# Optimization experiments

Measured on AMD Instinct MI355X. Metric: run time of the kernel, lower is better.

Reference implementation:

```python
import jax, jax.numpy as jnp
import numpy as np

K = 5            # adaptive kernel size
C = 256          # inplanes
M = 4
CM = C // M      # 64 bottleneck channels
PLANES = 256


def _depthwise_per_sample(f, w, b, dilation, pad):
    # f: [N, Cm, H, W]; w: [N, Cm, kh, kw] per-sample depthwise weights; b: [Cm]
    # Fold batch into the channel/group dim so one grouped conv does all samples.
    N, Cm, H, W = f.shape
    x = f.reshape(1, N * Cm, H, W)
    wk = w.reshape(N * Cm, 1, w.shape[2], w.shape[3])
    out = jax.lax.conv_general_dilated(
        x, wk, window_strides=(1, 1), padding=[(pad, pad), (pad, pad)],
        rhs_dilation=(dilation, dilation), feature_group_count=N * Cm,
        dimension_numbers=("NCHW", "OIHW", "NCHW"))
    return out.reshape(N, Cm, H, W) + b[None, :, None, None]


def setup_inputs() -> dict:
    key = jax.random.key(0)
    ks = jax.random.split(key, 16)
    N, H, W = 16, 96, 96
    s = 0.05
    return {
        "x": jax.random.normal(ks[0], (N, C, H, W), jnp.float32),
        "conv_w": jax.random.normal(ks[1], (CM, C)) * s,            # 1x1 conv C->Cm
        "conv_b": jax.random.normal(ks[2], (CM,)) * s,
        "conv_k_w": jax.random.normal(ks[3], ()) * s + 1.0,          # conv_k: 1x1, 1ch
        "conv_k_b": jax.random.normal(ks[4], ()) * s,
        "conv_k2_w": jax.random.normal(ks[5], ()) * s + 1.0,         # conv_k2
        "conv_k2_b": jax.random.normal(ks[6], ()) * s,
        "conv_kernel_w": jax.random.normal(ks[7], (K * K,)) * s,     # 1 -> k*k
        "conv_kernel_b": jax.random.normal(ks[8], (K * K,)) * s,
        "conv_kernel2_w": jax.random.normal(ks[9], (9,)) * s,        # 1 -> 9
        "conv_kernel2_b": jax.random.normal(ks[10], (9,)) * s,
        "fuse_w": jax.random.normal(ks[11], (PLANES // 2, CM)) * s,  # 1x1 fuse
        "fuse_b": jax.random.normal(ks[12], (PLANES // 2,)) * s,
        "adap_b": jax.random.normal(ks[13], (CM,)) * s,              # conv_adap_kernel.bias
        "atrous_b": jax.random.normal(ks[14], (CM,)) * s,            # conv3x3_atrous bias
    }


def reference(x, conv_w, conv_b, conv_k_w, conv_k_b, conv_k2_w, conv_k2_b,
              conv_kernel_w, conv_kernel_b, conv_kernel2_w, conv_kernel2_b,
              fuse_w, fuse_b, adap_b, atrous_b):
    N = x.shape[0]
    # f = relu(1x1 conv)
    f = jax.nn.relu(jnp.einsum("oc,nchw->nohw", conv_w, x) + conv_b[None, :, None, None])
    # g = relu(conv(avg_pool(x))) -> [N, Cm]
    g = jax.nn.relu(x.mean(axis=(2, 3)) @ conv_w.T + conv_b)
    # conv_kernel (1->k*k, 1x1) applied over the Cm "spatial" axis, then conv_k (scalar affine)
    # kernel[n,c,kk] = conv_k_w * (conv_kernel_w[kk]*g[n,c] + conv_kernel_b[kk]) + conv_k_b
    ker = conv_k_w * (g[:, :, None] * conv_kernel_w[None, None, :] + conv_kernel_b) + conv_k_b
    w_dyn = ker.reshape(N, CM, K, K)
    ker2 = conv_k2_w * (g[:, :, None] * conv_kernel2_w[None, None, :] + conv_kernel2_b) + conv_k2_b
    w_atr = ker2.reshape(N, CM, 3, 3)
    # per-sample dynamic depthwise convs
    out = _depthwise_per_sample(f, w_dyn, adap_b, dilation=1, pad=(K - 1) // 2)
    out_atr = _depthwise_per_sample(f, w_atr, atrous_b, dilation=2, pad=2)
    # fuse (1x1) each branch, concat on channels
    y = jnp.einsum("oc,nchw->nohw", fuse_w, out) + fuse_b[None, :, None, None]
    y_atr = jnp.einsum("oc,nchw->nohw", fuse_w, out_atr) + fuse_b[None, :, None, None]
    return jnp.concatenate([y, y_atr], axis=1)
```

## Files before the change

kernel.cpp:

```cpp
#include <hip/hip_runtime.h>
#include <hip/hip_bf16.h>
#include <stdint.h>

#define N_S   16
#define C_IN  256
#define CMID  64
#define HH    96
#define WW    96
#define HW    9216
#define PL2   128

#define CB_OFF   0
#define KW_OFF   64
#define KB_OFF   96
#define K2W_OFF  128
#define K2B_OFF  144
#define FB_OFF   160
#define AB_OFF   288
#define ATB_OFF  352
#define SC_OFF   416

typedef __attribute__((ext_vector_type(8))) short short8;
typedef __attribute__((ext_vector_type(4))) float floatx4;

__device__ __forceinline__ float ldbf(const uint16_t* p) {
    return __uint_as_float(((uint32_t)(*p)) << 16);
}
__device__ __forceinline__ uint16_t f2bf(float f) {
    __hip_bfloat16 h = __float2bfloat16(f);
    return *reinterpret_cast<uint16_t*>(&h);
}
__device__ __forceinline__ uint32_t pkbf(float lo, float hi) {
    return (uint32_t)f2bf(lo) | ((uint32_t)f2bf(hi) << 16);
}
__device__ __forceinline__ float bfsum2(uint32_t u) {
    return __uint_as_float(u << 16) + __uint_as_float(u & 0xffff0000u);
}

#define SWZ8(row) ((((row) ^ ((row) >> 3)) & 7) << 3)

__global__ __launch_bounds__(256) void k_prep(
    const uint16_t* __restrict__ xq,
    const void* conv_w, const void* conv_b, const void* ckw, const void* ckb,
    const void* ck2w, const void* ck2b, const void* kernw, const void* kernb,
    const void* kern2w, const void* kern2b, const void* fuse_w, const void* fuse_b,
    const void* adap_b, const void* atrous_b,
    int* __restrict__ flags,
    uint16_t* __restrict__ cw_bf, uint16_t* __restrict__ fw_bf,
    float* __restrict__ smalls) {
    __shared__ int cnt[2];
    int t = threadIdx.x;
    if (t < 2) cnt[t] = 0;
    __syncthreads();
    int cx = 0, cw = 0;
    const uint16_t* wq = (const uint16_t*)conv_w;
    for (int k = 0; k < 64; ++k) {
        uint16_t vx = xq[k * 256 + t];
        uint16_t vw = wq[k * 256 + t];
        if (((vx >> 7) & 0xFF) >= 0xC0) cx++;
        if (((vw >> 7) & 0xFF) >= 0xC0) cw++;
    }
    atomicAdd(&cnt[0], cx);
    atomicAdd(&cnt[1], cw);
    __syncthreads();
    bool f32 = cnt[1] > 64;
    if (blockIdx.x == 0 && t == 0) { flags[0] = cnt[0] > 64; flags[1] = f32; }

    for (int i = blockIdx.x * 256 + t; i < CMID * C_IN; i += 16 * 256)
        cw_bf[i] = f32 ? f2bf(((const float*)conv_w)[i]) : ((const uint16_t*)conv_w)[i];
    for (int i = blockIdx.x * 256 + t; i < PL2 * CMID; i += 16 * 256)
        fw_bf[i] = f32 ? f2bf(((const float*)fuse_w)[i]) : ((const uint16_t*)fuse_w)[i];
    if (blockIdx.x != 0) return;
    if (t < 64) {
        smalls[CB_OFF + t]  = f32 ? ((const float*)conv_b)[t]   : ldbf((const uint16_t*)conv_b + t);
        smalls[AB_OFF + t]  = f32 ? ((const float*)adap_b)[t]   : ldbf((const uint16_t*)adap_b + t);
        smalls[ATB_OFF + t] = f32 ? ((const float*)atrous_b)[t] : ldbf((const uint16_t*)atrous_b + t);
    }
    if (t < 128)
        smalls[FB_OFF + t] = f32 ? ((const float*)fuse_b)[t] : ldbf((const uint16_t*)fuse_b + t);
    if (t < 25) {
        smalls[KW_OFF + t] = f32 ? ((const float*)kernw)[t] : ldbf((const uint16_t*)kernw + t);
        smalls[KB_OFF + t] = f32 ? ((const float*)kernb)[t] : ldbf((const uint16_t*)kernb + t);
    }
    if (t < 9) {
        smalls[K2W_OFF + t] = f32 ? ((const float*)kern2w)[t] : ldbf((const uint16_t*)kern2w + t);
        smalls[K2B_OFF + t] = f32 ? ((const float*)kern2b)[t] : ldbf((const uint16_t*)kern2b + t);
    }
    if (t == 0) {
        smalls[SC_OFF + 0] = f32 ? ((const float*)ckw)[0]  : ldbf((const uint16_t*)ckw);
        smalls[SC_OFF + 1] = f32 ? ((const float*)ckb)[0]  : ldbf((const uint16_t*)ckb);
        smalls[SC_OFF + 2] = f32 ? ((const float*)ck2w)[0] : ldbf((const uint16_t*)ck2w);
        smalls[SC_OFF + 3] = f32 ? ((const float*)ck2b)[0] : ldbf((const uint16_t*)ck2b);
    }
}


#define ISSUE(cc, A0, A1, B0, B1) do {                                          \
    int c_ = (cc) * 64 + cp * 2;                                                \
    if (xf32) {                                                                 \
        const float* xb_ = (const float*)xv + ((size_t)n * C_IN + c_) * HW + px0;\
        A0 = *(const uint4*)xb_;        A1 = *(const uint4*)(xb_ + 4);          \
        B0 = *(const uint4*)(xb_ + HW); B1 = *(const uint4*)(xb_ + HW + 4);     \
    } else {                                                                    \
        const uint16_t* xb_ = (const uint16_t*)xv + ((size_t)n * C_IN + c_) * HW + px0;\
        A0 = *(const uint4*)xb_;        B0 = *(const uint4*)(xb_ + HW);         \
    }                                                                           \
} while (0)

#define CONVWRITE(cc, A0, A1, B0, B1) do {                                      \
    int c_ = (cc) * 64 + cp * 2;                                                \
    uint32_t pk_[8]; float s0_, s1_;                                            \
    if (xf32) {                                                                 \
        float av_[8], bw_[8];                                                   \
        av_[0] = __uint_as_float(A0.x); av_[1] = __uint_as_float(A0.y);         \
        av_[2] = __uint_as_float(A0.z); av_[3] = __uint_as_float(A0.w);         \
        av_[4] = __uint_as_float(A1.x); av_[5] = __uint_as_float(A1.y);         \
        av_[6] = __uint_as_float(A1.z); av_[7] = __uint_as_float(A1.w);         \
        bw_[0] = __uint_as_float(B0.x); bw_[1] = __uint_as_float(B0.y);         \
        bw_[2] = __uint_as_float(B0.z); bw_[3] = __uint_as_float(B0.w);         \
        bw_[4] = __uint_as_float(B1.x); bw_[5] = __uint_as_float(B1.y);         \
        bw_[6] = __uint_as_float(B1.z); bw_[7] = __uint_as_float(B1.w);         \
        s0_ = ((av_[0] + av_[1]) + (av_[2] + av_[3]))                           \
            + ((av_[4] + av_[5]) + (av_[6] + av_[7]));                          \
        s1_ = ((bw_[0] + bw_[1]) + (bw_[2] + bw_[3]))                           \
            + ((bw_[4] + bw_[5]) + (bw_[6] + bw_[7]));                          \
        _Pragma("unroll")                                                       \
        for (int j = 0; j < 8; ++j) pk_[j] = pkbf(av_[j], bw_[j]);              \
    } else {                                                                    \
        s0_ = (bfsum2(A0.x) + bfsum2(A0.y)) + (bfsum2(A0.z) + bfsum2(A0.w));    \
        s1_ = (bfsum2(B0.x) + bfsum2(B0.y)) + (bfsum2(B0.z) + bfsum2(B0.w));    \
        pk_[0] = (A0.x & 0xffffu) | (B0.x << 16);                               \
        pk_[1] = (A0.x >> 16)     | (B0.x & 0xffff0000u);                       \
        pk_[2] = (A0.y & 0xffffu) | (B0.y << 16);                               \
        pk_[3] = (A0.y >> 16)     | (B0.y & 0xffff0000u);                       \
        pk_[4] = (A0.z & 0xffffu) | (B0.z << 16);                               \
        pk_[5] = (A0.z >> 16)     | (B0.z & 0xffff0000u);                       \
        pk_[6] = (A0.w & 0xffffu) | (B0.w << 16);                               \
        pk_[7] = (A0.w >> 16)     | (B0.w & 0xffff0000u);                       \
    }                                                                           \
    int swz_ = pxg << 2;                                                        \
    _Pragma("unroll")                                                           \
    for (int j = 0; j < 8; ++j)                                                 \
        xl32[(pxg * 8 + j) * 36 + (cp ^ swz_)] = pk_[j];                        \
    s0_ += __shfl_xor(s0_, 4, 8); s0_ += __shfl_xor(s0_, 2, 8);                 \
    s0_ += __shfl_xor(s0_, 1, 8);                                               \
    s1_ += __shfl_xor(s1_, 4, 8); s1_ += __shfl_xor(s1_, 2, 8);                 \
    s1_ += __shfl_xor(s1_, 1, 8);                                               \
    if ((t & 7) == 0) *(float2*)(pbase + c_) = make_float2(s0_, s1_);           \
} while (0)

#define MFMA_PH(cc) do {                                                        \
    _Pragma("unroll")                                                           \
    for (int ks = 0; ks < 2; ++ks) {                                            \
        int kw_ = (cc) * 64 + ks * 32 + quad * 8;                               \
        const uint16_t* wp_ = cw_bf + kw_;                                      \
        short8 a0 = *(const short8*)(wp_ + (l16)      * 256);                   \
        short8 a1 = *(const short8*)(wp_ + (16 + l16) * 256);                   \
        short8 a2 = *(const short8*)(wp_ + (32 + l16) * 256);                   \
        short8 a3 = *(const short8*)(wp_ + (48 + l16) * 256);                   \
        int kdw_ = (ks * 16 + quad * 4) ^ ((pxw >> 3) << 2);                    \
        short8 bv = *(const short8*)(xl32 + (size_t)pxw * 36 + kdw_);           \
        acc[0] = __builtin_amdgcn_mfma_f32_16x16x32_bf16(a0, bv, acc[0], 0, 0, 0);\
        acc[1] = __builtin_amdgcn_mfma_f32_16x16x32_bf16(a1, bv, acc[1], 0, 0, 0);\
        acc[2] = __builtin_amdgcn_mfma_f32_16x16x32_bf16(a2, bv, acc[2], 0, 0, 0);\
        acc[3] = __builtin_amdgcn_mfma_f32_16x16x32_bf16(a3, bv, acc[3], 0, 0, 0);\
    }                                                                           \
} while (0)

__global__ __launch_bounds__(256) void k_conv1x1(
    const void* __restrict__ xv, const int* __restrict__ flags,
    const uint16_t* __restrict__ cw_bf, const float* __restrict__ smalls,
    uint16_t* __restrict__ fout, float* __restrict__ partials) {
    __shared__ uint16_t x_lds[64 * 72];
    int t = threadIdx.x;
    int b = blockIdx.x;
    int n = b / 144, blk = b % 144;
    int pxb = blk * 64;
    bool xf32 = flags[0] != 0;

    int lane = t & 63, wid = t >> 6;
    int l16 = lane & 15, quad = lane >> 4;
    int pxw = wid * 16 + l16;
    uint32_t* xl32 = (uint32_t*)x_lds;

    int pxg = t & 7, cp = t >> 3;
    int px0 = pxb + pxg * 8;

    floatx4 acc[4];
#pragma unroll
    for (int i = 0; i < 4; ++i) acc[i] = (floatx4){0.f, 0.f, 0.f, 0.f};

    float* pbase = partials + (size_t)(n * 144 + blk) * 256;

    uint4 pA0, pA1, pB0, pB1;
    uint4 qA0, qA1, qB0, qB1;

    ISSUE(0, pA0, pA1, pB0, pB1);
    ISSUE(1, qA0, qA1, qB0, qB1);
    CONVWRITE(0, pA0, pA1, pB0, pB1);
    ISSUE(2, pA0, pA1, pB0, pB1);
    __syncthreads();
    MFMA_PH(0);
    __syncthreads();
    CONVWRITE(1, qA0, qA1, qB0, qB1);
    ISSUE(3, qA0, qA1, qB0, qB1);
    __syncthreads();
    MFMA_PH(1);
    __syncthreads();
    CONVWRITE(2, pA0, pA1, pB0, pB1);
    __syncthreads();
    MFMA_PH(2);
    __syncthreads();
    CONVWRITE(3, qA0, qA1, qB0, qB1);
    __syncthreads();
    MFMA_PH(3);

#pragma unroll
    for (int mt = 0; mt < 4; ++mt) {
        int o = mt * 16 + quad * 4;
        float b0 = smalls[CB_OFF + o],     b1 = smalls[CB_OFF + o + 1];
        float b2 = smalls[CB_OFF + o + 2], b3 = smalls[CB_OFF + o + 3];
        float v0 = fmaxf(acc[mt][0] + b0, 0.f);
        float v1 = fmaxf(acc[mt][1] + b1, 0.f);
        float v2 = fmaxf(acc[mt][2] + b2, 0.f);
        float v3 = fmaxf(acc[mt][3] + b3, 0.f);
        *(uint2*)(x_lds + pxw * 72 + o) = make_uint2(pkbf(v0, v1), pkbf(v2, v3));
    }
    __syncthreads();
#pragma unroll
    for (int k = 0; k < 2; ++k) {
        int task = k * 256 + t;
        int o8 = (task & 7) * 8, pxl = task >> 3;
        *(uint4*)(fout + ((size_t)n * HW + pxb + pxl) * 64 + o8) =
            *(const uint4*)(x_lds + pxl * 72 + o8);
    }
}

__global__ __launch_bounds__(256) void k_weights2(
    const float* __restrict__ partials, const uint16_t* __restrict__ cw_bf,
    const float* __restrict__ smalls,
    float* __restrict__ w_dyn, float* __restrict__ w_atr) {
    __shared__ float s_sums[256];
    __shared__ float s_dot[256];
    int n = blockIdx.x, t = threadIdx.x;
    const float* pp = partials + (size_t)n * 144 * 256 + t;
    float s = 0.f;
#pragma unroll 8
    for (int k = 0; k < 144; ++k) s += pp[k * 256];
    s_sums[t] = s * (1.0f / (float)HW);
    __syncthreads();
    int cm = t & 63, seg = t >> 6;
    const uint16_t* wr = cw_bf + cm * 256 + seg * 64;
    const float* sr = s_sums + seg * 64;
    float acc = 0.f;
#pragma unroll 8
    for (int c = 0; c < 64; ++c) acc = fmaf(ldbf(wr + c), sr[c], acc);
    s_dot[t] = acc;
    __syncthreads();
    if (t < 64) {
        float a = s_dot[t] + s_dot[t + 64] + s_dot[t + 128] + s_dot[t + 192]
                + smalls[CB_OFF + t];
        float gv = fmaxf(a, 0.f);
        float ckw = smalls[SC_OFF + 0], ckb = smalls[SC_OFF + 1];
        float ck2w = smalls[SC_OFF + 2], ck2b = smalls[SC_OFF + 3];
        float* o1 = w_dyn + (size_t)(n * CMID + t) * 25;
#pragma unroll
        for (int k = 0; k < 25; ++k)
            o1[k] = fmaf(ckw, fmaf(gv, smalls[KW_OFF + k], smalls[KB_OFF + k]), ckb);
        float* o2 = w_atr + (size_t)(n * CMID + t) * 9;
#pragma unroll
        for (int k = 0; k < 9; ++k)
            o2[k] = fmaf(ck2w, fmaf(gv, smalls[K2W_OFF + k], smalls[K2B_OFF + k]), ck2b);
    }
}

__global__ __launch_bounds__(256) void k_dwfuse(
    const uint16_t* __restrict__ f,
    const float* __restrict__ w_dyn, const float* __restrict__ w_atr,
    const uint16_t* __restrict__ fw_bf, const float* __restrict__ smalls,
    float* __restrict__ out) {
    __shared__ uint16_t f_lds[160 * 64];
    __shared__ uint16_t d5_lds[64 * 72];
    __shared__ uint16_t dA_lds[64 * 72];

    int t = threadIdx.x;
    int orig = blockIdx.x;
    int b = (orig & 7) * 288 + (orig >> 3);
    int n = b / 144, tile = b % 144;
    int y0 = (tile / 6) * 4, x0 = (tile % 6) * 16;

    int c = t >> 2, q = t & 3;
    int qx = q << 2;
    float w5[25], w9[9];
    {
        const float* wp = w_dyn + (size_t)(n * CMID + c) * 25;
#pragma unroll
        for (int k = 0; k < 25; ++k) w5[k] = wp[k];
        const float* wa = w_atr + (size_t)(n * CMID + c) * 9;
#pragma unroll
        for (int k = 0; k < 9; ++k) w9[k] = wa[k];
    }

    const uint16_t* fbase = f + (size_t)n * HW * 64;
#pragma unroll
    for (int k = 0; k < 5; ++k) {
        int task = k * 256 + t;
        int row = task >> 3, c8 = (task & 7) * 8;
        int hy = row / 20, hx = row - hy * 20;
        int y = y0 - 2 + hy, xg = x0 - 2 + hx;
        uint4 v = make_uint4(0u, 0u, 0u, 0u);
        if (y >= 0 && y < HH && xg >= 0 && xg < WW)
            v = *(const uint4*)(fbase + ((size_t)y * WW + xg) * 64 + c8);
        *(uint4*)(f_lds + row * 64 + (c8 ^ SWZ8(row))) = v;
    }
    __syncthreads();

    {
        float p[8][8];
#pragma unroll
        for (int r = 0; r < 8; ++r)
#pragma unroll
            for (int cl = 0; cl < 8; ++cl) {
                int row = r * 20 + qx + cl;
                p[r][cl] = ldbf(f_lds + row * 64 + (c ^ SWZ8(row)));
            }

        float b5v = smalls[AB_OFF + c], bAv = smalls[ATB_OFF + c];
        float a5[4][4], aA[4][4];
#pragma unroll
        for (int i = 0; i < 4; ++i)
#pragma unroll
            for (int j = 0; j < 4; ++j) { a5[i][j] = b5v; aA[i][j] = bAv; }

#pragma unroll
        for (int i = 0; i < 5; ++i)
#pragma unroll
            for (int j = 0; j < 5; ++j) {
                float wv = w5[i * 5 + j];
#pragma unroll
                for (int oy = 0; oy < 4; ++oy)
#pragma unroll
                    for (int ox = 0; ox < 4; ++ox)
                        a5[oy][ox] = fmaf(wv, p[oy + i][ox + j], a5[oy][ox]);
            }
#pragma unroll
        for (int i = 0; i < 3; ++i)
#pragma unroll
            for (int j = 0; j < 3; ++j) {
                float wv = w9[i * 3 + j];
#pragma unroll
                for (int oy = 0; oy < 4; ++oy)
#pragma unroll
                    for (int ox = 0; ox < 4; ++ox)
                        aA[oy][ox] = fmaf(wv, p[oy + 2 * i][ox + 2 * j], aA[oy][ox]);
            }

#pragma unroll
        for (int oy = 0; oy < 4; ++oy)
#pragma unroll
            for (int ox = 0; ox < 4; ox += 2) {
                int px0 = oy * 16 + qx + ox;
                uint32_t p5 = pkbf(a5[oy][ox], a5[oy][ox + 1]);
                uint32_t pA = pkbf(aA[oy][ox], aA[oy][ox + 1]);
                d5_lds[px0 * 72 + c]       = (uint16_t)p5;
                d5_lds[(px0 + 1) * 72 + c] = (uint16_t)(p5 >> 16);
                dA_lds[px0 * 72 + c]       = (uint16_t)pA;
                dA_lds[(px0 + 1) * 72 + c] = (uint16_t)(pA >> 16);
            }
    }
    __syncthreads();

    {
        int lane = t & 63, wid = t >> 6;
        int l16 = lane & 15, quad = lane >> 4;
        const uint16_t* dl = (wid >= 2) ? dA_lds : d5_lds;
        int oh = (wid & 1) * 64;
        int obr = (wid >= 2) ? 128 : 0;

        floatx4 acc[4][4];
#pragma unroll
        for (int i = 0; i < 4; ++i)
#pragma unroll
            for (int j = 0; j < 4; ++j) acc[i][j] = (floatx4){0.f, 0.f, 0.f, 0.f};

#pragma unroll
        for (int ks = 0; ks < 2; ++ks) {
            int kk = ks * 32 + quad * 8;
            short8 a0 = *(const short8*)(dl + (l16)      * 72 + kk);
            short8 a1 = *(const short8*)(dl + (16 + l16) * 72 + kk);
            short8 a2 = *(const short8*)(dl + (32 + l16) * 72 + kk);
            short8 a3 = *(const short8*)(dl + (48 + l16) * 72 + kk);
#pragma unroll
            for (int nt = 0; nt < 4; ++nt) {
                short8 bv = *(const short8*)(fw_bf + (size_t)(oh + nt * 16 + l16) * 64 + kk);
                acc[0][nt] = __builtin_amdgcn_mfma_f32_16x16x32_bf16(a0, bv, acc[0][nt], 0, 0, 0);
                acc[1][nt] = __builtin_amdgcn_mfma_f32_16x16x32_bf16(a1, bv, acc[1][nt], 0, 0, 0);
                acc[2][nt] = __builtin_amdgcn_mfma_f32_16x16x32_bf16(a2, bv, acc[2][nt], 0, 0, 0);
                acc[3][nt] = __builtin_amdgcn_mfma_f32_16x16x32_bf16(a3, bv, acc[3][nt], 0, 0, 0);
            }
        }
#pragma unroll
        for (int nt = 0; nt < 4; ++nt) {
            int o = oh + nt * 16 + l16;
            float bias = smalls[FB_OFF + o];
            float* obp = out + ((size_t)(n * 256 + obr + o)) * HW + x0 + quad * 4;
#pragma unroll
            for (int mt = 0; mt < 4; ++mt) {
                float4 v;
                v.x = acc[mt][nt][0] + bias;
                v.y = acc[mt][nt][1] + bias;
                v.z = acc[mt][nt][2] + bias;
                v.w = acc[mt][nt][3] + bias;
                *(float4*)(obp + (size_t)(y0 + mt) * WW) = v;
            }
        }
    }
}

extern "C" void kernel_launch(void* const* d_in, const int* in_sizes, int n_in,
                              void* d_out, int out_size, void* d_ws, size_t ws_size,
                              hipStream_t stream) {
    float* out = (float*)d_out;

    char* ws = (char*)d_ws;
    int*      flags = (int*)ws;
    uint16_t* cw_bf = (uint16_t*)(ws + 256);
    uint16_t* fw_bf = (uint16_t*)(ws + 33024);
    float*    smalls = (float*)(ws + 49408);
    float*    partials = (float*)(ws + 65536);
    float*    w_dyn = (float*)(ws + 2424832);
    float*    w_atr = (float*)(ws + 2527232);
    uint16_t* f     = (uint16_t*)(ws + 2564096);

    k_prep<<<dim3(16), dim3(256), 0, stream>>>(
        (const uint16_t*)d_in[0],
        d_in[1], d_in[2], d_in[3], d_in[4], d_in[5], d_in[6], d_in[7], d_in[8],
        d_in[9], d_in[10], d_in[11], d_in[12], d_in[13], d_in[14],
        flags, cw_bf, fw_bf, smalls);
    k_conv1x1<<<dim3(N_S * 144), dim3(256), 0, stream>>>(
        d_in[0], flags, cw_bf, smalls, f, partials);
    k_weights2<<<dim3(N_S), dim3(256), 0, stream>>>(
        partials, cw_bf, smalls, w_dyn, w_atr);
    k_dwfuse<<<dim3(N_S * 144), dim3(256), 0, stream>>>(
        f, w_dyn, w_atr, fw_bf, smalls, out);
}
```

Measured before the change: 368.3 us.

## Double-buffer conv1x1 LDS staging and stream depthwise rows to cut registers

The 1x1 conv kernel now ping-pongs between two LDS buffers for successive 64-channel chunks, which removes half of the barriers between the conversion writes and the MFMA reads. The depthwise+fuse kernel processes the halo tile one row at a time instead of holding an 8x8 patch in registers. It also reuses the input LDS region for the depthwise output buffers, with an extra barrier, and sets launch bounds asking for 5 blocks per CU. Together these aim to improve occupancy and overlap, at the cost of more LDS in the first kernel and an extra sync in the second.

```diff
diff --git a/kernel.cpp b/kernel.cpp
--- a/kernel.cpp
+++ b/kernel.cpp
@@ -107,7 +107,7 @@
     }                                                                           \
 } while (0)
 
-#define CONVWRITE(cc, A0, A1, B0, B1) do {                                      \
+#define CONVWRITE(cc, A0, A1, B0, B1, XL) do {                                  \
     int c_ = (cc) * 64 + cp * 2;                                                \
     uint32_t pk_[8]; float s0_, s1_;                                            \
     if (xf32) {                                                                 \
@@ -141,7 +141,7 @@
     int swz_ = pxg << 2;                                                        \
     _Pragma("unroll")                                                           \
     for (int j = 0; j < 8; ++j)                                                 \
-        xl32[(pxg * 8 + j) * 36 + (cp ^ swz_)] = pk_[j];                        \
+        (XL)[(pxg * 8 + j) * 36 + (cp ^ swz_)] = pk_[j];                        \
     s0_ += __shfl_xor(s0_, 4, 8); s0_ += __shfl_xor(s0_, 2, 8);                 \
     s0_ += __shfl_xor(s0_, 1, 8);                                               \
     s1_ += __shfl_xor(s1_, 4, 8); s1_ += __shfl_xor(s1_, 2, 8);                 \
@@ -149,7 +149,7 @@
     if ((t & 7) == 0) *(float2*)(pbase + c_) = make_float2(s0_, s1_);           \
 } while (0)
 
-#define MFMA_PH(cc) do {                                                        \
+#define MFMA_PH(cc, XL) do {                                                    \
     _Pragma("unroll")                                                           \
     for (int ks = 0; ks < 2; ++ks) {                                            \
         int kw_ = (cc) * 64 + ks * 32 + quad * 8;                               \
@@ -159,7 +159,7 @@
         short8 a2 = *(const short8*)(wp_ + (32 + l16) * 256);                   \
         short8 a3 = *(const short8*)(wp_ + (48 + l16) * 256);                   \
         int kdw_ = (ks * 16 + quad * 4) ^ ((pxw >> 3) << 2);                    \
-        short8 bv = *(const short8*)(xl32 + (size_t)pxw * 36 + kdw_);           \
+        short8 bv = *(const short8*)((XL) + (size_t)pxw * 36 + kdw_);           \
         acc[0] = __builtin_amdgcn_mfma_f32_16x16x32_bf16(a0, bv, acc[0], 0, 0, 0);\
         acc[1] = __builtin_amdgcn_mfma_f32_16x16x32_bf16(a1, bv, acc[1], 0, 0, 0);\
         acc[2] = __builtin_amdgcn_mfma_f32_16x16x32_bf16(a2, bv, acc[2], 0, 0, 0);\
@@ -171,7 +171,7 @@
     const void* __restrict__ xv, const int* __restrict__ flags,
     const uint16_t* __restrict__ cw_bf, const float* __restrict__ smalls,
     uint16_t* __restrict__ fout, float* __restrict__ partials) {
-    __shared__ uint16_t x_lds[64 * 72];
+    __shared__ uint16_t x_lds[2 * 64 * 72];
     int t = threadIdx.x;
     int b = blockIdx.x;
     int n = b / 144, blk = b % 144;
@@ -181,7 +181,8 @@
     int lane = t & 63, wid = t >> 6;
     int l16 = lane & 15, quad = lane >> 4;
     int pxw = wid * 16 + l16;
-    uint32_t* xl32 = (uint32_t*)x_lds;
+    uint32_t* xb0 = (uint32_t*)x_lds;
+    uint32_t* xb1 = xb0 + 2304;
 
     int pxg = t & 7, cp = t >> 3;
     int px0 = pxb + pxg * 8;
@@ -196,24 +197,21 @@
     uint4 qA0, qA1, qB0, qB1;
 
     ISSUE(0, pA0, pA1, pB0, pB1);
+    CONVWRITE(0, pA0, pA1, pB0, pB1, xb0);
     ISSUE(1, qA0, qA1, qB0, qB1);
-    CONVWRITE(0, pA0, pA1, pB0, pB1);
+    __syncthreads();
+    MFMA_PH(0, xb0);
+    CONVWRITE(1, qA0, qA1, qB0, qB1, xb1);
     ISSUE(2, pA0, pA1, pB0, pB1);
     __syncthreads();
-    MFMA_PH(0);
-    __syncthreads();
-    CONVWRITE(1, qA0, qA1, qB0, qB1);
+    MFMA_PH(1, xb1);
+    CONVWRITE(2, pA0, pA1, pB0, pB1, xb0);
     ISSUE(3, qA0, qA1, qB0, qB1);
     __syncthreads();
-    MFMA_PH(1);
-    __syncthreads();
-    CONVWRITE(2, pA0, pA1, pB0, pB1);
-    __syncthreads();
-    MFMA_PH(2);
-    __syncthreads();
-    CONVWRITE(3, qA0, qA1, qB0, qB1);
-    __syncthreads();
-    MFMA_PH(3);
+    MFMA_PH(2, xb0);
+    CONVWRITE(3, qA0, qA1, qB0, qB1, xb1);
+    __syncthreads();
+    MFMA_PH(3, xb1);
 
 #pragma unroll
     for (int mt = 0; mt < 4; ++mt) {
@@ -274,14 +272,14 @@
     }
 }
 
-__global__ __launch_bounds__(256) void k_dwfuse(
+__global__ __launch_bounds__(256, 5) void k_dwfuse(
     const uint16_t* __restrict__ f,
     const float* __restrict__ w_dyn, const float* __restrict__ w_atr,
     const uint16_t* __restrict__ fw_bf, const float* __restrict__ smalls,
     float* __restrict__ out) {
-    __shared__ uint16_t f_lds[160 * 64];
-    __shared__ uint16_t d5_lds[64 * 72];
-    __shared__ uint16_t dA_lds[64 * 72];
+    __shared__ uint16_t u_lds[160 * 64];
+    uint16_t* d5_lds = u_lds;
+    uint16_t* dA_lds = u_lds + 64 * 72;
 
     int t = threadIdx.x;
     int orig = blockIdx.x;
@@ -311,63 +309,63 @@
         uint4 v = make_uint4(0u, 0u, 0u, 0u);
         if (y >= 0 && y < HH && xg >= 0 && xg < WW)
             v = *(const uint4*)(fbase + ((size_t)y * WW + xg) * 64 + c8);
-        *(uint4*)(f_lds + row * 64 + (c8 ^ SWZ8(row))) = v;
-    }
-    __syncthreads();
-
-    {
-        float p[8][8];
-#pragma unroll
-        for (int r = 0; r < 8; ++r)
-#pragma unroll
-            for (int cl = 0; cl < 8; ++cl) {
-                int row = r * 20 + qx + cl;
-                p[r][cl] = ldbf(f_lds + row * 64 + (c ^ SWZ8(row)));
+        *(uint4*)(u_lds + row * 64 + (c8 ^ SWZ8(row))) = v;
+    }
+    __syncthreads();
+
+    float b5v = smalls[AB_OFF + c], bAv = smalls[ATB_OFF + c];
+    float a5[4][4], aA[4][4];
+#pragma unroll
+    for (int i = 0; i < 4; ++i)
+#pragma unroll
+        for (int j = 0; j < 4; ++j) { a5[i][j] = b5v; aA[i][j] = bAv; }
+
+#pragma unroll
+    for (int r = 0; r < 8; ++r) {
+        float row[8];
+#pragma unroll
+        for (int cl = 0; cl < 8; ++cl) {
+            int rw = r * 20 + qx + cl;
+            row[cl] = ldbf(u_lds + rw * 64 + (c ^ SWZ8(rw)));
+        }
+#pragma unroll
+        for (int oy = 0; oy < 4; ++oy) {
+            int d = r - oy;
+            if (d >= 0 && d <= 4) {
+#pragma unroll
+                for (int j = 0; j < 5; ++j) {
+                    float wv = w5[d * 5 + j];
+#pragma unroll
+                    for (int ox = 0; ox < 4; ++ox)
+                        a5[oy][ox] = fmaf(wv, row[ox + j], a5[oy][ox]);
+                }
             }
-
-        float b5v = smalls[AB_OFF + c], bAv = smalls[ATB_OFF + c];
-        float a5[4][4], aA[4][4];
-#pragma unroll
-        for (int i = 0; i < 4; ++i)
-#pragma unroll
-            for (int j = 0; j < 4; ++j) { a5[i][j] = b5v; aA[i][j] = bAv; }
-
-#pragma unroll
-        for (int i = 0; i < 5; ++i)
-#pragma unroll
-            for (int j = 0; j < 5; ++j) {
-                float wv = w5[i * 5 + j];
-#pragma unroll
-                for (int oy = 0; oy < 4; ++oy)
+            if (d >= 0 && d <= 4 && (d & 1) == 0) {
+                int i2 = d >> 1;
+#pragma unroll
+                for (int j = 0; j < 3; ++j) {
+                    float wv = w9[i2 * 3 + j];
 #pragma unroll
                     for (int ox = 0; ox < 4; ++ox)
-                        a5[oy][ox] = fmaf(wv, p[oy + i][ox + j], a5[oy][ox]);
+                        aA[oy][ox] = fmaf(wv, row[ox + 2 * j], aA[oy][ox]);
+                }
             }
-#pragma unroll
-        for (int i = 0; i < 3; ++i)
-#pragma unroll
-            for (int j = 0; j < 3; ++j) {
-                float wv = w9[i * 3 + j];
-#pragma unroll
-                for (int oy = 0; oy < 4; ++oy)
-#pragma unroll
-                    for (int ox = 0; ox < 4; ++ox)
-                        aA[oy][ox] = fmaf(wv, p[oy + 2 * i][ox + 2 * j], aA[oy][ox]);
-            }
-
-#pragma unroll
-        for (int oy = 0; oy < 4; ++oy)
-#pragma unroll
-            for (int ox = 0; ox < 4; ox += 2) {
-                int px0 = oy * 16 + qx + ox;
-                uint32_t p5 = pkbf(a5[oy][ox], a5[oy][ox + 1]);
-                uint32_t pA = pkbf(aA[oy][ox], aA[oy][ox + 1]);
-                d5_lds[px0 * 72 + c]       = (uint16_t)p5;
-                d5_lds[(px0 + 1) * 72 + c] = (uint16_t)(p5 >> 16);
-                dA_lds[px0 * 72 + c]       = (uint16_t)pA;
-                dA_lds[(px0 + 1) * 72 + c] = (uint16_t)(pA >> 16);
-            }
-    }
+        }
+    }
+    __syncthreads();
+
+#pragma unroll
+    for (int oy = 0; oy < 4; ++oy)
+#pragma unroll
+        for (int ox = 0; ox < 4; ox += 2) {
+            int pxo = oy * 16 + qx + ox;
+            uint32_t p5 = pkbf(a5[oy][ox], a5[oy][ox + 1]);
+            uint32_t pA = pkbf(aA[oy][ox], aA[oy][ox + 1]);
+            d5_lds[pxo * 72 + c]       = (uint16_t)p5;
+            d5_lds[(pxo + 1) * 72 + c] = (uint16_t)(p5 >> 16);
+            dA_lds[pxo * 72 + c]       = (uint16_t)pA;
+            dA_lds[(pxo + 1) * 72 + c] = (uint16_t)(pA >> 16);
+        }
     __syncthreads();
 
     {
```

New measurement: 404.3 us. 9.8% more time.
